# Optimization experiments

Measured on AMD Instinct MI355X. Metric: run time of the kernel, lower is better.

## Reference

```python
import math
import jax, jax.numpy as jnp
import numpy as np

D = 1536      # d_model
H = 12        # n_heads
L = 12        # n_layers
V = 50257     # vocab (hardcoded in module)
P = 1024      # max positions (hardcoded)
B = 1         # batch (must be 1: pos-embed uses arange(len(idx)))
S = 1024      # sequence length


def setup_inputs() -> dict:
    key = jax.random.key(0)
    ks = jax.random.split(key, 10)
    sc = 0.02
    n = lambda k, shape: (jax.random.normal(k, shape, jnp.float32) * sc)
    return {
        "idx": jax.random.randint(ks[0], (B, S), 0, V),
        "mask": jnp.tril(jnp.ones((S, S), jnp.int32)),  # causal mask
        "tok_emb": n(ks[1], (V, D)),
        "pos_emb": n(ks[2], (P, D)),
        "Wqkv": n(ks[3], (L, D, 3 * D)), "bqkv": jnp.zeros((L, 3 * D), jnp.float32),
        "Wo":   n(ks[4], (L, D, D)),     "bo":   jnp.zeros((L, D), jnp.float32),
        "W1":   n(ks[5], (L, D, 4 * D)), "b1":   jnp.zeros((L, 4 * D), jnp.float32),
        "W2":   n(ks[6], (L, 4 * D, D)), "b2":   jnp.zeros((L, D), jnp.float32),
        "ln_g": jnp.ones((D,), jnp.float32), "ln_b": jnp.zeros((D,), jnp.float32),
        "Wout": n(ks[7], (D, D)), "bout": jnp.zeros((D,), jnp.float32),
    }


def _gpt_forward(idx, mask, tok_emb, pos_emb, Wqkv, bqkv, Wo, bo,
                 W1, b1, W2, b2, ln_g, ln_b, Wout, bout):
    b, s = idx.shape
    d = tok_emb.shape[1]
    hd = d // H
    scale = 1.0 / math.sqrt(d)  # note: module divides by sqrt(d_model), not head_dim

    # faithful quirk: position_embedding(arange(len(idx))) -> (B, D), broadcasts since B==1
    x = tok_emb[idx] + pos_emb[:b]  # (B,S,D)

    mask0 = (mask == 0)  # (S,S) -> broadcast over (B,H,S,S)

    def block(x, p):
        wqkv, bqkv_, wo, bo_, w1, b1_, w2, b2_ = p
        qkv = x @ wqkv + bqkv_                       # (B,S,3D)
        q, k, v = jnp.split(qkv, 3, axis=-1)
        q = q.reshape(b, s, H, hd)
        k = k.reshape(b, s, H, hd)
        v = v.reshape(b, s, H, hd)
        scores = jnp.einsum('bqhd,bkhd->bhqk', q, k) * scale
        scores = jnp.where(mask0, -jnp.inf, scores)
        attn = jax.nn.softmax(scores, axis=-2)       # non-standard: softmax over QUERY axis
        o = jnp.einsum('bhqk,bkhd->bqhd', attn, v).reshape(b, s, d)
        x = x + (o @ wo + bo_)                       # attention residual
        x = x + (jax.nn.relu(x @ w1 + b1_) @ w2 + b2_)  # FFN residual (on post-attn x)
        return x, None

    x, _ = jax.lax.scan(block, x, (Wqkv, bqkv, Wo, bo, W1, b1, W2, b2))

    # final LayerNorm (eps=1e-5 like torch default)
    mu = jnp.mean(x, axis=-1, keepdims=True)
    var = jnp.mean(jnp.square(x - mu), axis=-1, keepdims=True)
    xn = (x - mu) * jax.lax.rsqrt(var + 1e-5) * ln_g + ln_b
    return xn @ Wout + bout


def reference(idx, mask, tok_emb, pos_emb, Wqkv, bqkv, Wo, bo,
              W1, b1, W2, b2, ln_g, ln_b, Wout, bout):
    return _gpt_forward(idx, mask, tok_emb, pos_emb, Wqkv, bqkv, Wo, bo,
                        W1, b1, W2, b2, ln_g, ln_b, Wout, bout)
```

## Files before the change

### kernel.cpp

```cpp
#include <hip/hip_runtime.h>
#include <stdint.h>
#include <math.h>

#define D_MODEL 1536
#define NH 12
#define HD 128
#define NL 12
#define SEQ 1024
#define D3 4608
#define D4 6144
#define SCALE 0.025515518153991442f

typedef __attribute__((ext_vector_type(8))) short short8;
typedef __attribute__((ext_vector_type(4))) float floatx4;

__device__ __forceinline__ uint32_t packhi(float a, float b) {
  return (__float_as_uint(a) >> 16) | (__float_as_uint(b) & 0xFFFF0000u);
}
__device__ __forceinline__ float truncf32(float a) {
  return __uint_as_float(__float_as_uint(a) & 0xFFFF0000u);
}
__device__ __forceinline__ void split8v(float4 v0, float4 v1, uint4 &hi, uint4 &lo) {
  hi.x = packhi(v0.x, v0.y); hi.y = packhi(v0.z, v0.w);
  hi.z = packhi(v1.x, v1.y); hi.w = packhi(v1.z, v1.w);
  lo.x = packhi(v0.x - truncf32(v0.x), v0.y - truncf32(v0.y));
  lo.y = packhi(v0.z - truncf32(v0.z), v0.w - truncf32(v0.w));
  lo.z = packhi(v1.x - truncf32(v1.x), v1.y - truncf32(v1.y));
  lo.w = packhi(v1.z - truncf32(v1.z), v1.w - truncf32(v1.w));
}

__device__ __forceinline__ int xcd_chunk_id(int nwg) {
  int orig = blockIdx.x;
  int xcd = orig & 7, pos = orig >> 3;
  int q = nwg >> 3, r = nwg & 7;
  return (xcd < r ? xcd * (q + 1) : r * (q + 1) + (xcd - r) * q) + pos;
}

__global__ __launch_bounds__(256)
void embed_kernel(const int* __restrict__ idx, const float* __restrict__ tok,
                  const float* __restrict__ pos, float* __restrict__ x) {
  int i = blockIdx.x * 256 + threadIdx.x;
  int s = i / D_MODEL;
  int d = i - s * D_MODEL;
  x[i] = tok[(size_t)idx[s] * D_MODEL + d] + pos[d];
}

template<int BM, bool RELU, bool RES, int SPLITK, bool TA2>
__global__ __launch_bounds__(256)
void mgemm_kernel(const float* __restrict__ A, const float* __restrict__ Ab,
                  const float* __restrict__ B,
                  const float* __restrict__ bias, const float* __restrict__ res,
                  float* __restrict__ C, int M, int N, int K, int NC, int NR) {
  constexpr int MI = BM / 32;
  constexpr int AE = BM / 8;
  constexpr int TPR = 32 / AE;
  __shared__ short Ah[2][BM][36], Al[2][BM][36];
  __shared__ short Bh[2][128][36], Bl[2][128][36];
  const int tid = threadIdx.x;
  const int lane = tid & 63, wave = tid >> 6;

  const int lid = xcd_chunk_id(NC * NR * SPLITK);
  const int z   = lid / (NC * NR);
  const int rem = lid - z * (NC * NR);
  const int ct  = rem / NR;
  const int rt  = rem - ct * NR;
  const int bm = rt * BM, bn = ct << 7;

  const int wm = (wave >> 1) * (BM / 2), wn = (wave & 1) << 6;
  const int fr = lane & 15, fk = (lane >> 4) << 3;
  const int Kc = K / SPLITK;
  const int kbase = (SPLITK > 1) ? z * Kc : 0;

  floatx4 acc[MI][4];
#pragma unroll
  for (int i = 0; i < MI; i++)
#pragma unroll
    for (int j = 0; j < 4; j++) acc[i][j] = (floatx4){0.f, 0.f, 0.f, 0.f};

  const int ar = tid / TPR;
  const int ac = (tid % TPR) * AE;
  const int bc = tid & 127;
  const int bkq = (tid >> 7) << 4;
  const float* Ag  = A + (size_t)(bm + ar) * K + kbase + ac;
  const float* Ag2 = TA2 ? (Ab + (size_t)(bm + ar) * K + kbase + ac) : nullptr;
  const float* Bg = B + (size_t)(kbase + bkq) * N + bn + bc;

  float a_reg[AE];
  float b_reg[16];

  auto LOADG = [&](int k0) {
#pragma unroll
    for (int e = 0; e < AE / 4; e++) {
      float4 v = *(const float4*)(Ag + k0 + 4 * e);
      if constexpr (TA2) {
        float4 w = *(const float4*)(Ag2 + k0 + 4 * e);
        v.x += w.x; v.y += w.y; v.z += w.z; v.w += w.w;
      }
      a_reg[4 * e + 0] = v.x; a_reg[4 * e + 1] = v.y;
      a_reg[4 * e + 2] = v.z; a_reg[4 * e + 3] = v.w;
    }
    const float* Bp = Bg + (size_t)k0 * N;
#pragma unroll
    for (int j = 0; j < 16; j++) b_reg[j] = Bp[(size_t)j * N];
  };
  auto STORE = [&](int buf) {
#pragma unroll
    for (int e = 0; e < AE / 8; e++) {
      float4 v0 = {a_reg[8 * e + 0], a_reg[8 * e + 1], a_reg[8 * e + 2], a_reg[8 * e + 3]};
      float4 v1 = {a_reg[8 * e + 4], a_reg[8 * e + 5], a_reg[8 * e + 6], a_reg[8 * e + 7]};
      uint4 hi, lo; split8v(v0, v1, hi, lo);
      *(uint4*)&Ah[buf][ar][ac + 8 * e] = hi;
      *(uint4*)&Al[buf][ar][ac + 8 * e] = lo;
    }
#pragma unroll
    for (int e = 0; e < 2; e++) {
      float4 u0 = {b_reg[8 * e + 0], b_reg[8 * e + 1], b_reg[8 * e + 2], b_reg[8 * e + 3]};
      float4 u1 = {b_reg[8 * e + 4], b_reg[8 * e + 5], b_reg[8 * e + 6], b_reg[8 * e + 7]};
      uint4 hi, lo; split8v(u0, u1, hi, lo);
      *(uint4*)&Bh[buf][bc][bkq + 8 * e] = hi;
      *(uint4*)&Bl[buf][bc][bkq + 8 * e] = lo;
    }
  };

  LOADG(0);
  STORE(0);
  __syncthreads();

  for (int k0 = 0; k0 < Kc; k0 += 32) {
    const int cur = (k0 >> 5) & 1;
    const bool more = (k0 + 32 < Kc);
    if (more) LOADG(k0 + 32);

    short8 ah[MI], al[MI], bh[4], bl[4];
#pragma unroll
    for (int i = 0; i < MI; i++) {
      ah[i] = *(const short8*)&Ah[cur][wm + (i << 4) + fr][fk];
      al[i] = *(const short8*)&Al[cur][wm + (i << 4) + fr][fk];
    }
#pragma unroll
    for (int j = 0; j < 4; j++) {
      bh[j] = *(const short8*)&Bh[cur][wn + (j << 4) + fr][fk];
      bl[j] = *(const short8*)&Bl[cur][wn + (j << 4) + fr][fk];
    }
#pragma unroll
    for (int i = 0; i < MI; i++)
#pragma unroll
      for (int j = 0; j < 4; j++) {
        acc[i][j] = __builtin_amdgcn_mfma_f32_16x16x32_bf16(ah[i], bh[j], acc[i][j], 0, 0, 0);
        acc[i][j] = __builtin_amdgcn_mfma_f32_16x16x32_bf16(ah[i], bl[j], acc[i][j], 0, 0, 0);
        acc[i][j] = __builtin_amdgcn_mfma_f32_16x16x32_bf16(al[i], bh[j], acc[i][j], 0, 0, 0);
      }

    if (more) STORE(cur ^ 1);
    __syncthreads();
  }

  const int cr = (lane >> 4) << 2, cc = lane & 15;
  if constexpr (SPLITK > 1) {
    float* Cp = C + (size_t)z * M * N;
#pragma unroll
    for (int j = 0; j < 4; j++) {
      const int col = bn + wn + (j << 4) + cc;
#pragma unroll
      for (int i = 0; i < MI; i++) {
        const int row0 = bm + wm + (i << 4) + cr;
#pragma unroll
        for (int r = 0; r < 4; r++)
          Cp[(size_t)(row0 + r) * N + col] = acc[i][j][r];
      }
    }
  } else {
#pragma unroll
    for (int j = 0; j < 4; j++) {
      const int col = bn + wn + (j << 4) + cc;
      const float bv = bias[col];
#pragma unroll
      for (int i = 0; i < MI; i++) {
        const int row0 = bm + wm + (i << 4) + cr;
#pragma unroll
        for (int r = 0; r < 4; r++) {
          float v = acc[i][j][r] + bv;
          if constexpr (RES) v += res[(size_t)(row0 + r) * N + col];
          if constexpr (RELU) v = fmaxf(v, 0.f);
          C[(size_t)(row0 + r) * N + col] = v;
        }
      }
    }
  }
}

template<bool HASB, bool RES, bool RELU>
__global__ __launch_bounds__(256)
void combine_kernel(const float* __restrict__ p0, const float* __restrict__ p1,
                    const float* __restrict__ bias, const float* __restrict__ res,
                    float* __restrict__ C, int N) {
  const int i = (blockIdx.x * 256 + threadIdx.x) << 2;
  float4 a = *(const float4*)&p0[i];
  float4 b = *(const float4*)&p1[i];
  float4 r = {a.x + b.x, a.y + b.y, a.z + b.z, a.w + b.w};
  if constexpr (HASB) {
    const int col = i % N;
    float4 bv = *(const float4*)&bias[col];
    r.x += bv.x; r.y += bv.y; r.z += bv.z; r.w += bv.w;
  }
  if constexpr (RES) {
    float4 rv = *(const float4*)&res[i];
    r.x += rv.x; r.y += rv.y; r.z += rv.z; r.w += rv.w;
  }
  if constexpr (RELU) {
    r.x = fmaxf(r.x, 0.f); r.y = fmaxf(r.y, 0.f);
    r.z = fmaxf(r.z, 0.f); r.w = fmaxf(r.w, 0.f);
  }
  *(float4*)&C[i] = r;
}

__global__ __launch_bounds__(256)
void scores_kernel(const float* __restrict__ qkv, float* __restrict__ scores,
                   float* __restrict__ pstats) {
  __shared__ short Qh[128][40], Ql[128][40], Kh[128][40], Kl[128][40];
  const int tid = threadIdx.x;
  const int lane = tid & 63, wave = tid >> 6;

  const int lid = xcd_chunk_id(NH * 36);
  const int h = lid / 36;
  int t = lid - h * 36;
  int rr = 0;
  while ((rr + 1) * (rr + 2) / 2 <= t) rr++;
  const int bi = rr << 7;
  const int bj = (t - rr * (rr + 1) / 2) << 7;

  const int wm = (wave >> 1) << 6, wn = (wave & 1) << 6;
  const int fr = lane & 15, fk = (lane >> 4) << 3;
  const float* Q = qkv + h * HD;
  const float* Kp = qkv + D_MODEL + h * HD;

  floatx4 acc[4][4];
#pragma unroll
  for (int i = 0; i < 4; i++)
#pragma unroll
    for (int j = 0; j < 4; j++) acc[i][j] = (floatx4){0.f, 0.f, 0.f, 0.f};

  const int ar = tid >> 1;
  const int ac = (tid & 1) << 4;

  for (int k0 = 0; k0 < HD; k0 += 32) {
    __syncthreads();
    {
      const float* Qp = Q + (size_t)(bi + ar) * D3 + k0 + ac;
#pragma unroll
      for (int e = 0; e < 2; e++) {
        float4 v0 = *(const float4*)(Qp + 8 * e);
        float4 v1 = *(const float4*)(Qp + 8 * e + 4);
        uint4 hi, lo; split8v(v0, v1, hi, lo);
        *(uint4*)&Qh[ar][ac + 8 * e] = hi;
        *(uint4*)&Ql[ar][ac + 8 * e] = lo;
      }
      const float* Kpp = Kp + (size_t)(bj + ar) * D3 + k0 + ac;
#pragma unroll
      for (int e = 0; e < 2; e++) {
        float4 v0 = *(const float4*)(Kpp + 8 * e);
        float4 v1 = *(const float4*)(Kpp + 8 * e + 4);
        uint4 hi, lo; split8v(v0, v1, hi, lo);
        *(uint4*)&Kh[ar][ac + 8 * e] = hi;
        *(uint4*)&Kl[ar][ac + 8 * e] = lo;
      }
    }
    __syncthreads();
    short8 qh[4], ql[4], kh[4], kl[4];
#pragma unroll
    for (int i = 0; i < 4; i++) {
      qh[i] = *(const short8*)&Qh[wm + (i << 4) + fr][fk];
      ql[i] = *(const short8*)&Ql[wm + (i << 4) + fr][fk];
      kh[i] = *(const short8*)&Kh[wn + (i << 4) + fr][fk];
      kl[i] = *(const short8*)&Kl[wn + (i << 4) + fr][fk];
    }
#pragma unroll
    for (int i = 0; i < 4; i++)
#pragma unroll
      for (int j = 0; j < 4; j++) {
        acc[i][j] = __builtin_amdgcn_mfma_f32_16x16x32_bf16(qh[i], kh[j], acc[i][j], 0, 0, 0);
        acc[i][j] = __builtin_amdgcn_mfma_f32_16x16x32_bf16(qh[i], kl[j], acc[i][j], 0, 0, 0);
        acc[i][j] = __builtin_amdgcn_mfma_f32_16x16x32_bf16(ql[i], kh[j], acc[i][j], 0, 0, 0);
        acc[i][j] = __builtin_amdgcn_mfma_f32_16x16x32_bf16(ql[i], kl[j], acc[i][j], 0, 0, 0);
      }
  }

  const int cr = (lane >> 4) << 2, cc = lane & 15;
  float* S = scores + (size_t)h * SEQ * SEQ;
  const int qc = (bi >> 6) + (wave >> 1);
  float* Pm = pstats + (size_t)((h * 16 + qc) * 2 + 0) * 1024;
  float* Pz = pstats + (size_t)((h * 16 + qc) * 2 + 1) * 1024;
#pragma unroll
  for (int j = 0; j < 4; j++) {
    const int col = bj + wn + (j << 4) + cc;
    float vv[16];
    float m = -1e30f;
#pragma unroll
    for (int i = 0; i < 4; i++) {
      const int row0 = bi + wm + (i << 4) + cr;
#pragma unroll
      for (int r = 0; r < 4; r++) {
        float v = (col <= row0 + r) ? acc[i][j][r] * SCALE : -1e30f;
        S[(size_t)(row0 + r) * SEQ + col] = v;
        vv[i * 4 + r] = v;
        m = fmaxf(m, v);
      }
    }
    float zz = 0.f;
#pragma unroll
    for (int t2 = 0; t2 < 16; t2++) zz += __expf(vv[t2] - m);
    if (m == -1e30f) zz = 0.f;
#pragma unroll
    for (int off = 16; off <= 32; off <<= 1) {
      float mo = __shfl_xor(m, off, 64);
      float zo = __shfl_xor(zz, off, 64);
      float mn = fmaxf(m, mo);
      zz = zz * __expf(m - mn) + zo * __expf(mo - mn);
      m = mn;
    }
    if ((lane >> 4) == 0) { Pm[col] = m; Pz[col] = zz; }
  }
}

__global__ __launch_bounds__(256)
void av_kernel(const float* __restrict__ qkv, const float* __restrict__ scores,
               const float* __restrict__ pstats, float* __restrict__ part) {
  __shared__ short Ph[64][40], Pl[64][40], Vh[128][40], Vl[128][40];
  __shared__ float Ms[512], Rs[512];
  const int tid = threadIdx.x;
  const int lane = tid & 63, wave = tid >> 6;

  const int lid = xcd_chunk_id(NH * 32);
  const int h = lid >> 5;
  const int t = lid & 31;
  const int y = t >> 1, z = t & 1;
  const int bm = y << 6;

  const int wm = (wave >> 1) << 5, wn = (wave & 1) << 6;
  const int fr = lane & 15, fk = (lane >> 4) << 3;
  const float* S = scores + (size_t)h * SEQ * SEQ;
  const float* V = qkv + 2 * D_MODEL + h * HD;

  const int kbeg = z * (y + 1) * 32;
  const int kend = (z + 1) * (y + 1) * 32;
  const int ncols = kend - kbeg;

  for (int c0 = tid; c0 < ncols; c0 += 256) {
    const int c = kbeg + c0;
    const int q0 = c >> 6;
    float m = -1e30f;
    for (int qc = q0; qc < 16; qc++)
      m = fmaxf(m, pstats[(size_t)((h * 16 + qc) * 2 + 0) * 1024 + c]);
    float zz = 0.f;
    for (int qc = q0; qc < 16; qc++) {
      float pm = pstats[(size_t)((h * 16 + qc) * 2 + 0) * 1024 + c];
      float pz = pstats[(size_t)((h * 16 + qc) * 2 + 1) * 1024 + c];
      zz += pz * __expf(pm - m);
    }
    Ms[c0] = m;
    Rs[c0] = 1.f / zz;
  }

  floatx4 acc[2][4];
#pragma unroll
  for (int i = 0; i < 2; i++)
#pragma unroll
    for (int j = 0; j < 4; j++) acc[i][j] = (floatx4){0.f, 0.f, 0.f, 0.f};

  const int ar = tid >> 2;
  const int ac = (tid & 3) << 3;
  const int bc = tid & 127;
  const int bkq = (tid >> 7) << 4;

  for (int k0 = kbeg; k0 < kend; k0 += 32) {
    __syncthreads();
    {
      const float* Sp = S + (size_t)(bm + ar) * SEQ + k0 + ac;
      float4 v0 = *(const float4*)(Sp);
      float4 v1 = *(const float4*)(Sp + 4);
      float t8[8] = {v0.x, v0.y, v0.z, v0.w, v1.x, v1.y, v1.z, v1.w};
      float4 p0, p1;
      {
        int kk = k0 - kbeg + ac;
        p0.x = __expf(t8[0] - Ms[kk + 0]) * Rs[kk + 0];
        p0.y = __expf(t8[1] - Ms[kk + 1]) * Rs[kk + 1];
        p0.z = __expf(t8[2] - Ms[kk + 2]) * Rs[kk + 2];
        p0.w = __expf(t8[3] - Ms[kk + 3]) * Rs[kk + 3];
        p1.x = __expf(t8[4] - Ms[kk + 4]) * Rs[kk + 4];
        p1.y = __expf(t8[5] - Ms[kk + 5]) * Rs[kk + 5];
        p1.z = __expf(t8[6] - Ms[kk + 6]) * Rs[kk + 6];
        p1.w = __expf(t8[7] - Ms[kk + 7]) * Rs[kk + 7];
      }
      uint4 hi, lo; split8v(p0, p1, hi, lo);
      *(uint4*)&Ph[ar][ac] = hi;
      *(uint4*)&Pl[ar][ac] = lo;
    }
    {
      const float* Vp = V + (size_t)(k0 + bkq) * D3 + bc;
#pragma unroll
      for (int e = 0; e < 2; e++) {
        float4 u0, u1;
        u0.x = Vp[(size_t)(8 * e + 0) * D3]; u0.y = Vp[(size_t)(8 * e + 1) * D3];
        u0.z = Vp[(size_t)(8 * e + 2) * D3]; u0.w = Vp[(size_t)(8 * e + 3) * D3];
        u1.x = Vp[(size_t)(8 * e + 4) * D3]; u1.y = Vp[(size_t)(8 * e + 5) * D3];
        u1.z = Vp[(size_t)(8 * e + 6) * D3]; u1.w = Vp[(size_t)(8 * e + 7) * D3];
        uint4 hi, lo; split8v(u0, u1, hi, lo);
        *(uint4*)&Vh[bc][bkq + 8 * e] = hi;
        *(uint4*)&Vl[bc][bkq + 8 * e] = lo;
      }
    }
    __syncthreads();
    short8 ph[2], pl[2], vh[4], vl[4];
#pragma unroll
    for (int i = 0; i < 2; i++) {
      ph[i] = *(const short8*)&Ph[wm + (i << 4) + fr][fk];
      pl[i] = *(const short8*)&Pl[wm + (i << 4) + fr][fk];
    }
#pragma unroll
    for (int j = 0; j < 4; j++) {
      vh[j] = *(const short8*)&Vh[wn + (j << 4) + fr][fk];
      vl[j] = *(const short8*)&Vl[wn + (j << 4) + fr][fk];
    }
#pragma unroll
    for (int i = 0; i < 2; i++)
#pragma unroll
      for (int j = 0; j < 4; j++) {
        acc[i][j] = __builtin_amdgcn_mfma_f32_16x16x32_bf16(ph[i], vh[j], acc[i][j], 0, 0, 0);
        acc[i][j] = __builtin_amdgcn_mfma_f32_16x16x32_bf16(ph[i], vl[j], acc[i][j], 0, 0, 0);
        acc[i][j] = __builtin_amdgcn_mfma_f32_16x16x32_bf16(pl[i], vh[j], acc[i][j], 0, 0, 0);
      }
  }

  const int cr = (lane >> 4) << 2, cc = lane & 15;
  float* Cp = part + (size_t)z * SEQ * D_MODEL;
#pragma unroll
  for (int j = 0; j < 4; j++) {
    const int col = h * HD + wn + (j << 4) + cc;
#pragma unroll
    for (int i = 0; i < 2; i++) {
      const int row0 = bm + wm + (i << 4) + cr;
#pragma unroll
      for (int r = 0; r < 4; r++)
        Cp[(size_t)(row0 + r) * D_MODEL + col] = acc[i][j][r];
    }
  }
}

__global__ __launch_bounds__(256)
void ln_kernel(const float* __restrict__ x, const float* __restrict__ g,
               const float* __restrict__ bb, float* __restrict__ y) {
  __shared__ float red[8];
  const int row = blockIdx.x;
  const float* xr = x + (size_t)row * D_MODEL;
  float v[6];
  float s = 0.f, sq = 0.f;
#pragma unroll
  for (int i = 0; i < 6; i++) {
    v[i] = xr[256 * i + threadIdx.x];
    s += v[i];
    sq += v[i] * v[i];
  }
#pragma unroll
  for (int off = 32; off >= 1; off >>= 1) {
    s += __shfl_down(s, off, 64);
    sq += __shfl_down(sq, off, 64);
  }
  const int lane = threadIdx.x & 63, w = threadIdx.x >> 6;
  if (lane == 0) { red[w] = s; red[4 + w] = sq; }
  __syncthreads();
  if (threadIdx.x == 0) {
    red[0] = red[0] + red[1] + red[2] + red[3];
    red[4] = red[4] + red[5] + red[6] + red[7];
  }
  __syncthreads();
  const float mu = red[0] * (1.f / D_MODEL);
  const float var = red[4] * (1.f / D_MODEL) - mu * mu;
  const float rs = rsqrtf(var + 1e-5f);
#pragma unroll
  for (int i = 0; i < 6; i++) {
    int c = 256 * i + threadIdx.x;
    y[(size_t)row * D_MODEL + c] = (v[i] - mu) * rs * g[c] + bb[c];
  }
}

extern "C" void kernel_launch(void* const* d_in, const int* in_sizes, int n_in,
                              void* d_out, int out_size, void* d_ws, size_t ws_size,
                              hipStream_t stream) {
  (void)in_sizes; (void)n_in; (void)out_size; (void)ws_size;
  const int*   idx     = (const int*)d_in[0];
  const float* tok_emb = (const float*)d_in[2];
  const float* pos_emb = (const float*)d_in[3];
  const float* Wqkv    = (const float*)d_in[4];
  const float* bqkv    = (const float*)d_in[5];
  const float* Wo      = (const float*)d_in[6];
  const float* bo      = (const float*)d_in[7];
  const float* W1      = (const float*)d_in[8];
  const float* b1      = (const float*)d_in[9];
  const float* W2      = (const float*)d_in[10];
  const float* b2      = (const float*)d_in[11];
  const float* ln_g    = (const float*)d_in[12];
  const float* ln_b    = (const float*)d_in[13];
  const float* Wout    = (const float*)d_in[14];
  const float* bout    = (const float*)d_in[15];
  float* out = (float*)d_out;

  char* ws = (char*)d_ws;
  float* x      = (float*)(ws);
  float* qkv    = (float*)(ws + 6291456);
  float* pstats = (float*)(ws + 25165824);
  float* part   = (float*)(ws + 26836992);
  float* U      = (float*)(ws + 52002816);
  float* scores = U;
  float* h1     = U;
  float* xn     = U;
  const size_t PN = (size_t)SEQ * D_MODEL;

  embed_kernel<<<6144, 256, 0, stream>>>(idx, tok_emb, pos_emb, x);

  for (int l = 0; l < NL; l++) {
    const float* wqkv = Wqkv + (size_t)l * D_MODEL * D3;
    const float* bq   = bqkv + (size_t)l * D3;
    const float* wo   = Wo   + (size_t)l * D_MODEL * D_MODEL;
    const float* bo_  = bo   + (size_t)l * D_MODEL;
    const float* w1   = W1   + (size_t)l * D_MODEL * D4;
    const float* b1_  = b1   + (size_t)l * D4;
    const float* w2   = W2   + (size_t)l * D4 * D_MODEL;
    const float* b2_  = b2   + (size_t)l * D_MODEL;

    mgemm_kernel<128, false, false, 1, false><<<288, 256, 0, stream>>>(
        x, nullptr, wqkv, bq, nullptr, qkv, SEQ, D3, D_MODEL, 36, 8);
    scores_kernel<<<432, 256, 0, stream>>>(qkv, scores, pstats);
    av_kernel<<<384, 256, 0, stream>>>(qkv, scores, pstats, part);
    mgemm_kernel<64, false, false, 2, true><<<384, 256, 0, stream>>>(
        part, part + PN, wo, nullptr, nullptr, part + 2 * PN,
        SEQ, D_MODEL, D_MODEL, 12, 16);
    combine_kernel<true, true, false><<<1536, 256, 0, stream>>>(
        part + 2 * PN, part + 3 * PN, bo_, x, x, D_MODEL);
    mgemm_kernel<128, true, false, 1, false><<<384, 256, 0, stream>>>(
        x, nullptr, w1, b1_, nullptr, h1, SEQ, D4, D_MODEL, 48, 8);
    mgemm_kernel<64, false, false, 2, false><<<384, 256, 0, stream>>>(
        h1, nullptr, w2, nullptr, nullptr, part, SEQ, D_MODEL, D4, 12, 16);
    combine_kernel<true, true, false><<<1536, 256, 0, stream>>>(
        part, part + PN, b2_, x, x, D_MODEL);
  }

  ln_kernel<<<SEQ, 256, 0, stream>>>(x, ln_g, ln_b, xn);
  mgemm_kernel<64, false, false, 2, false><<<384, 256, 0, stream>>>(
      xn, nullptr, Wout, nullptr, nullptr, part, SEQ, D_MODEL, D_MODEL, 12, 16);
  combine_kernel<true, false, false><<<1536, 256, 0, stream>>>(
      part, part + PN, bout, nullptr, out, D_MODEL);
}
```

Baseline: 5.060 ms.

## Switch GEMM to 128x64 tiles and drop LDS double buffering

Replaces the templated BM x 128 tile GEMM with a fixed 128x64 output tile, so each wave computes 64x32 and B loads shrink to 8 values per thread. The double-buffered shared-memory pipeline, where the next tile's global load overlapped the MFMA work, becomes a single buffer with two barriers per K step. Launch grids double for the QKV and FFN1 GEMMs and change shape for the split-K GEMMs. The goal is more blocks, higher occupancy and a smaller LDS footprint, at the cost of lost load/compute overlap and less reuse per tile.

```diff
diff --git a/kernel.cpp b/kernel.cpp
--- a/kernel.cpp
+++ b/kernel.cpp
@@ -45,17 +45,14 @@
   x[i] = tok[(size_t)idx[s] * D_MODEL + d] + pos[d];
 }
 
-template<int BM, bool RELU, bool RES, int SPLITK, bool TA2>
+template<bool RELU, bool RES, int SPLITK, bool TA2>
 __global__ __launch_bounds__(256)
 void mgemm_kernel(const float* __restrict__ A, const float* __restrict__ Ab,
                   const float* __restrict__ B,
                   const float* __restrict__ bias, const float* __restrict__ res,
                   float* __restrict__ C, int M, int N, int K, int NC, int NR) {
-  constexpr int MI = BM / 32;
-  constexpr int AE = BM / 8;
-  constexpr int TPR = 32 / AE;
-  __shared__ short Ah[2][BM][36], Al[2][BM][36];
-  __shared__ short Bh[2][128][36], Bl[2][128][36];
+  __shared__ short Ah[128][36], Al[128][36];
+  __shared__ short Bh[64][36], Bl[64][36];
   const int tid = threadIdx.x;
   const int lane = tid & 63, wave = tid >> 6;
 
@@ -64,33 +61,33 @@
   const int rem = lid - z * (NC * NR);
   const int ct  = rem / NR;
   const int rt  = rem - ct * NR;
-  const int bm = rt * BM, bn = ct << 7;
-
-  const int wm = (wave >> 1) * (BM / 2), wn = (wave & 1) << 6;
+  const int bm = rt << 7, bn = ct << 6;
+
+  const int wm = (wave >> 1) << 6, wn = (wave & 1) << 5;
   const int fr = lane & 15, fk = (lane >> 4) << 3;
   const int Kc = K / SPLITK;
   const int kbase = (SPLITK > 1) ? z * Kc : 0;
 
-  floatx4 acc[MI][4];
-#pragma unroll
-  for (int i = 0; i < MI; i++)
-#pragma unroll
-    for (int j = 0; j < 4; j++) acc[i][j] = (floatx4){0.f, 0.f, 0.f, 0.f};
-
-  const int ar = tid / TPR;
-  const int ac = (tid % TPR) * AE;
-  const int bc = tid & 127;
-  const int bkq = (tid >> 7) << 4;
+  floatx4 acc[4][2];
+#pragma unroll
+  for (int i = 0; i < 4; i++)
+#pragma unroll
+    for (int j = 0; j < 2; j++) acc[i][j] = (floatx4){0.f, 0.f, 0.f, 0.f};
+
+  const int ar = tid >> 1;
+  const int ac = (tid & 1) << 4;
+  const int bc = tid & 63;
+  const int bkq = (tid >> 6) << 3;
   const float* Ag  = A + (size_t)(bm + ar) * K + kbase + ac;
   const float* Ag2 = TA2 ? (Ab + (size_t)(bm + ar) * K + kbase + ac) : nullptr;
   const float* Bg = B + (size_t)(kbase + bkq) * N + bn + bc;
 
-  float a_reg[AE];
-  float b_reg[16];
-
-  auto LOADG = [&](int k0) {
-#pragma unroll
-    for (int e = 0; e < AE / 4; e++) {
+  float a_reg[16];
+  float b_reg[8];
+
+  for (int k0 = 0; k0 < Kc; k0 += 32) {
+#pragma unroll
+    for (int e = 0; e < 4; e++) {
       float4 v = *(const float4*)(Ag + k0 + 4 * e);
       if constexpr (TA2) {
         float4 w = *(const float4*)(Ag2 + k0 + 4 * e);
@@ -99,70 +96,58 @@
       a_reg[4 * e + 0] = v.x; a_reg[4 * e + 1] = v.y;
       a_reg[4 * e + 2] = v.z; a_reg[4 * e + 3] = v.w;
     }
-    const float* Bp = Bg + (size_t)k0 * N;
-#pragma unroll
-    for (int j = 0; j < 16; j++) b_reg[j] = Bp[(size_t)j * N];
-  };
-  auto STORE = [&](int buf) {
-#pragma unroll
-    for (int e = 0; e < AE / 8; e++) {
+    {
+      const float* Bp = Bg + (size_t)k0 * N;
+#pragma unroll
+      for (int j = 0; j < 8; j++) b_reg[j] = Bp[(size_t)j * N];
+    }
+    __syncthreads();
+#pragma unroll
+    for (int e = 0; e < 2; e++) {
       float4 v0 = {a_reg[8 * e + 0], a_reg[8 * e + 1], a_reg[8 * e + 2], a_reg[8 * e + 3]};
       float4 v1 = {a_reg[8 * e + 4], a_reg[8 * e + 5], a_reg[8 * e + 6], a_reg[8 * e + 7]};
       uint4 hi, lo; split8v(v0, v1, hi, lo);
-      *(uint4*)&Ah[buf][ar][ac + 8 * e] = hi;
-      *(uint4*)&Al[buf][ar][ac + 8 * e] = lo;
-    }
-#pragma unroll
-    for (int e = 0; e < 2; e++) {
-      float4 u0 = {b_reg[8 * e + 0], b_reg[8 * e + 1], b_reg[8 * e + 2], b_reg[8 * e + 3]};
-      float4 u1 = {b_reg[8 * e + 4], b_reg[8 * e + 5], b_reg[8 * e + 6], b_reg[8 * e + 7]};
+      *(uint4*)&Ah[ar][ac + 8 * e] = hi;
+      *(uint4*)&Al[ar][ac + 8 * e] = lo;
+    }
+    {
+      float4 u0 = {b_reg[0], b_reg[1], b_reg[2], b_reg[3]};
+      float4 u1 = {b_reg[4], b_reg[5], b_reg[6], b_reg[7]};
       uint4 hi, lo; split8v(u0, u1, hi, lo);
-      *(uint4*)&Bh[buf][bc][bkq + 8 * e] = hi;
-      *(uint4*)&Bl[buf][bc][bkq + 8 * e] = lo;
-    }
-  };
-
-  LOADG(0);
-  STORE(0);
-  __syncthreads();
-
-  for (int k0 = 0; k0 < Kc; k0 += 32) {
-    const int cur = (k0 >> 5) & 1;
-    const bool more = (k0 + 32 < Kc);
-    if (more) LOADG(k0 + 32);
-
-    short8 ah[MI], al[MI], bh[4], bl[4];
-#pragma unroll
-    for (int i = 0; i < MI; i++) {
-      ah[i] = *(const short8*)&Ah[cur][wm + (i << 4) + fr][fk];
-      al[i] = *(const short8*)&Al[cur][wm + (i << 4) + fr][fk];
-    }
-#pragma unroll
-    for (int j = 0; j < 4; j++) {
-      bh[j] = *(const short8*)&Bh[cur][wn + (j << 4) + fr][fk];
-      bl[j] = *(const short8*)&Bl[cur][wn + (j << 4) + fr][fk];
-    }
-#pragma unroll
-    for (int i = 0; i < MI; i++)
-#pragma unroll
-      for (int j = 0; j < 4; j++) {
+      *(uint4*)&Bh[bc][bkq] = hi;
+      *(uint4*)&Bl[bc][bkq] = lo;
+    }
+    __syncthreads();
+
+    short8 ah[4], al[4], bh[2], bl[2];
+#pragma unroll
+    for (int i = 0; i < 4; i++) {
+      ah[i] = *(const short8*)&Ah[wm + (i << 4) + fr][fk];
+      al[i] = *(const short8*)&Al[wm + (i << 4) + fr][fk];
+    }
+#pragma unroll
+    for (int j = 0; j < 2; j++) {
+      bh[j] = *(const short8*)&Bh[wn + (j << 4) + fr][fk];
+      bl[j] = *(const short8*)&Bl[wn + (j << 4) + fr][fk];
+    }
+#pragma unroll
+    for (int i = 0; i < 4; i++)
+#pragma unroll
+      for (int j = 0; j < 2; j++) {
         acc[i][j] = __builtin_amdgcn_mfma_f32_16x16x32_bf16(ah[i], bh[j], acc[i][j], 0, 0, 0);
         acc[i][j] = __builtin_amdgcn_mfma_f32_16x16x32_bf16(ah[i], bl[j], acc[i][j], 0, 0, 0);
         acc[i][j] = __builtin_amdgcn_mfma_f32_16x16x32_bf16(al[i], bh[j], acc[i][j], 0, 0, 0);
       }
-
-    if (more) STORE(cur ^ 1);
-    __syncthreads();
   }
 
   const int cr = (lane >> 4) << 2, cc = lane & 15;
   if constexpr (SPLITK > 1) {
     float* Cp = C + (size_t)z * M * N;
 #pragma unroll
-    for (int j = 0; j < 4; j++) {
+    for (int j = 0; j < 2; j++) {
       const int col = bn + wn + (j << 4) + cc;
 #pragma unroll
-      for (int i = 0; i < MI; i++) {
+      for (int i = 0; i < 4; i++) {
         const int row0 = bm + wm + (i << 4) + cr;
 #pragma unroll
         for (int r = 0; r < 4; r++)
@@ -171,11 +156,11 @@
     }
   } else {
 #pragma unroll
-    for (int j = 0; j < 4; j++) {
+    for (int j = 0; j < 2; j++) {
       const int col = bn + wn + (j << 4) + cc;
       const float bv = bias[col];
 #pragma unroll
-      for (int i = 0; i < MI; i++) {
+      for (int i = 0; i < 4; i++) {
         const int row0 = bm + wm + (i << 4) + cr;
 #pragma unroll
         for (int r = 0; r < 4; r++) {
@@ -527,26 +512,26 @@
     const float* w2   = W2   + (size_t)l * D4 * D_MODEL;
     const float* b2_  = b2   + (size_t)l * D_MODEL;
 
-    mgemm_kernel<128, false, false, 1, false><<<288, 256, 0, stream>>>(
-        x, nullptr, wqkv, bq, nullptr, qkv, SEQ, D3, D_MODEL, 36, 8);
+    mgemm_kernel<false, false, 1, false><<<576, 256, 0, stream>>>(
+        x, nullptr, wqkv, bq, nullptr, qkv, SEQ, D3, D_MODEL, 72, 8);
     scores_kernel<<<432, 256, 0, stream>>>(qkv, scores, pstats);
     av_kernel<<<384, 256, 0, stream>>>(qkv, scores, pstats, part);
-    mgemm_kernel<64, false, false, 2, true><<<384, 256, 0, stream>>>(
+    mgemm_kernel<false, false, 2, true><<<384, 256, 0, stream>>>(
         part, part + PN, wo, nullptr, nullptr, part + 2 * PN,
-        SEQ, D_MODEL, D_MODEL, 12, 16);
+        SEQ, D_MODEL, D_MODEL, 24, 8);
     combine_kernel<true, true, false><<<1536, 256, 0, stream>>>(
         part + 2 * PN, part + 3 * PN, bo_, x, x, D_MODEL);
-    mgemm_kernel<128, true, false, 1, false><<<384, 256, 0, stream>>>(
-        x, nullptr, w1, b1_, nullptr, h1, SEQ, D4, D_MODEL, 48, 8);
-    mgemm_kernel<64, false, false, 2, false><<<384, 256, 0, stream>>>(
-        h1, nullptr, w2, nullptr, nullptr, part, SEQ, D_MODEL, D4, 12, 16);
+    mgemm_kernel<true, false, 1, false><<<768, 256, 0, stream>>>(
+        x, nullptr, w1, b1_, nullptr, h1, SEQ, D4, D_MODEL, 96, 8);
+    mgemm_kernel<false, false, 2, false><<<384, 256, 0, stream>>>(
+        h1, nullptr, w2, nullptr, nullptr, part, SEQ, D_MODEL, D4, 24, 8);
     combine_kernel<true, true, false><<<1536, 256, 0, stream>>>(
         part, part + PN, b2_, x, x, D_MODEL);
   }
 
   ln_kernel<<<SEQ, 256, 0, stream>>>(x, ln_g, ln_b, xn);
-  mgemm_kernel<64, false, false, 2, false><<<384, 256, 0, stream>>>(
-      xn, nullptr, Wout, nullptr, nullptr, part, SEQ, D_MODEL, D_MODEL, 12, 16);
+  mgemm_kernel<false, false, 2, false><<<384, 256, 0, stream>>>(
+      xn, nullptr, Wout, nullptr, nullptr, part, SEQ, D_MODEL, D_MODEL, 24, 8);
   combine_kernel<true, false, false><<<1536, 256, 0, stream>>>(
       part, part + PN, bout, nullptr, out, D_MODEL);
 }
```

Measured after the change: 4.725 ms. 6.6% less time.
